# Performance work log

Measured on AMD Instinct MI355X. Metric: run time of the kernel, lower is better.

## Reference

```python
import jax, jax.numpy as jnp
import numpy as np

N_UPDATE = 3

def _lin(key, fan_in, fan_out):
    s = 1.0 / np.sqrt(fan_in)
    k1, k2 = jax.random.split(key)
    W = jax.random.uniform(k1, (fan_in, fan_out), jnp.float32, -s, s)
    b = jax.random.uniform(k2, (fan_out,), jnp.float32, -s, s)
    return W, b

def setup_inputs() -> dict:
    key = jax.random.key(0)
    ks = jax.random.split(key, 12)
    N, E, F_NODE, F_EDGE, H, L, R, T = 50000, 400000, 16, 16, 32, 64, 128, 1
    inp = {}
    inp["x"] = jax.random.normal(ks[0], (N, F_NODE), jnp.float32)
    inp["edge_index"] = jax.random.randint(ks[1], (E, 2), 0, N)  # [E,2] (src,dst)
    inp["edge_attr"] = jax.random.normal(ks[2], (E, F_EDGE), jnp.float32)
    # edge MLP: F_EDGE -> 64 -> 64 -> H*H
    inp["Wm0"], inp["bm0"] = _lin(ks[3], F_EDGE, L)
    inp["Wm1"], inp["bm1"] = _lin(ks[4], L, L)
    inp["Wm2"], inp["bm2"] = _lin(ks[5], L, H * H)
    # NNConv root weight + bias
    inp["root"], inp["bias"] = _lin(ks[6], H, H)
    # readout i-net: 2H -> R -> T ; j-net: H -> R -> T
    inp["Wi0"], inp["bi0"] = _lin(ks[7], 2 * H, R)
    inp["Wi1"], inp["bi1"] = _lin(ks[8], R, T)
    inp["Wj0"], inp["bj0"] = _lin(ks[9], H, R)
    inp["Wj1"], inp["bj1"] = _lin(ks[10], R, T)
    return inp

def reference(x, edge_index, edge_attr, Wm0, bm0, Wm1, bm1, Wm2, bm2,
              root, bias, Wi0, bi0, Wi1, bi1, Wj0, bj0, Wj1, bj1):
    N = x.shape[0]
    H = root.shape[0]
    # h_0 = [x, zeros] padded to hidden_state_size
    h0 = jnp.concatenate([x, jnp.zeros((N, H - x.shape[1]), x.dtype)], axis=1)
    # edge MLP -> per-edge weight matrices (edge_attr constant across updates)
    e = jax.nn.relu(edge_attr @ Wm0 + bm0)
    e = jax.nn.relu(e @ Wm1 + bm1)
    W = (e @ Wm2 + bm2).reshape(-1, H, H)  # [E, H, H]
    src = edge_index[:, 0]
    dst = edge_index[:, 1]
    h = h0
    for _ in range(N_UPDATE):
        msg = jnp.einsum('eh,eho->eo', h[src], W)              # gather + bmm
        agg = jax.ops.segment_sum(msg, dst, num_segments=N)    # scatter-add
        h = h @ root + bias + agg                              # NNConv root/bias
    # mpnn readout: sum_v sigmoid(i([h_T, h_0])) * j(h_T)
    gate = jax.nn.sigmoid(jax.nn.relu(jnp.concatenate([h, h0], 1) @ Wi0 + bi0) @ Wi1 + bi1)
    val = jax.nn.relu(h @ Wj0 + bj0) @ Wj1 + bj1
    return jnp.sum(gate * val, axis=0)  # [target_size]
```

## Files before the change

### kernel.cpp

```cpp
#include <hip/hip_runtime.h>
#include <stdint.h>

#define N_UPDATE 3
#define HD 32
#define FN 16

typedef unsigned short u16;
typedef __bf16 bf16x8 __attribute__((ext_vector_type(8)));
typedef float f32x4 __attribute__((ext_vector_type(4)));

__device__ __forceinline__ float bf2f(u16 u) {
  union { uint32_t i; float f; } v; v.i = ((uint32_t)u) << 16; return v.f;
}
__device__ __forceinline__ u16 f2bf(float f) {
  union { uint32_t i; float f; } v; v.f = f;
  uint32_t x = v.i;
  return (u16)((x + 0x7fffu + ((x >> 16) & 1u)) >> 16);
}

union frag16 { uint4 v; bf16x8 b; u16 s[8]; };

__global__ void k_zero_i(int* __restrict__ p, int n) {
  int i = blockIdx.x * blockDim.x + threadIdx.x;
  if (i < n) p[i] = 0;
}

__global__ void k_hist2(const int* __restrict__ eidx, int* __restrict__ cntS,
                        int* __restrict__ cntD, int E) {
  int e = blockIdx.x * blockDim.x + threadIdx.x;
  if (e >= E) return;
  int2 sd = ((const int2*)eidx)[e];
  atomicAdd(&cntS[sd.x], 1);
  atomicAdd(&cntD[sd.y], 1);
}

__global__ __launch_bounds__(1024) void k_scan(const int* __restrict__ cnt,
                                               int* __restrict__ out1,
                                               int* __restrict__ out2, int N) {
  __shared__ int sums[1024];
  int chunk = (N + 1023) / 1024;
  int beg = threadIdx.x * chunk;
  int end = beg + chunk; if (end > N) end = N;
  if (beg > N) beg = N;
  int s = 0;
  for (int i = beg; i < end; i++) s += cnt[i];
  sums[threadIdx.x] = s;
  __syncthreads();
  for (int off = 1; off < 1024; off <<= 1) {
    int v = (threadIdx.x >= off) ? sums[threadIdx.x - off] : 0;
    __syncthreads();
    sums[threadIdx.x] += v;
    __syncthreads();
  }
  int run = (threadIdx.x == 0) ? 0 : sums[threadIdx.x - 1];
  for (int i = beg; i < end; i++) {
    out1[i] = run;
    if (out2) out2[i] = run;
    run += cnt[i];
  }
  if (end == N) {
    out1[N] = run;
    if (out2) out2[N] = run;
  }
}

__global__ void k_scatter_src(const int* __restrict__ eidx, int* __restrict__ ptrS,
                              int* __restrict__ se_src, int* __restrict__ se_dst,
                              int* __restrict__ invp, int E) {
  int e = blockIdx.x * blockDim.x + threadIdx.x;
  if (e >= E) return;
  int2 sd = ((const int2*)eidx)[e];
  int pos = atomicAdd(&ptrS[sd.x], 1);
  se_src[pos] = sd.x;
  se_dst[pos] = sd.y;
  invp[e] = pos;
}

__global__ void k_dstpos(const int* __restrict__ se_dst, int* __restrict__ ptrD,
                         int* __restrict__ dstpos, int E) {
  int q = blockIdx.x * blockDim.x + threadIdx.x;
  if (q >= E) return;
  dstpos[q] = atomicAdd(&ptrD[se_dst[q]], 1);
}

__global__ void k_prep_bf(const float* __restrict__ Wm2, uint4* __restrict__ Bf) {
  int t = blockIdx.x;
  int lane = threadIdx.x;
  int col = lane & 15;
  int hg = lane >> 4;
  int p = t >> 6;
  int t2 = t & 63;
  int j2 = t2 * 16 + col;
  int o = p * 16 + (j2 >> 6);
  int k = j2 & 63;
  frag16 f;
#pragma unroll
  for (int jj = 0; jj < 8; jj++) {
    int h = hg * 8 + jj;
    f.s[jj] = f2bf(Wm2[k * 1024 + h * 32 + o]);
  }
  Bf[t * 64 + lane] = f.v;
}

__global__ void k_init_h(const float* __restrict__ x, const float* __restrict__ bm2,
                         float* __restrict__ h, float* __restrict__ hbbuf, int N) {
  int idx = blockIdx.x * blockDim.x + threadIdx.x;
  if (idx >= N * HD) return;
  int n = idx >> 5, o = idx & 31;
  float v = (o < FN) ? x[n * FN + o] : 0.f;
  h[idx] = v;
  float hb = 0.f;
#pragma unroll
  for (int k = 0; k < 32; k++)
    hb = fmaf(__shfl(v, k, 32), bm2[k * 32 + o], hb);
  hbbuf[idx] = hb;
}

__global__ __launch_bounds__(256) void k_edge_mlp(
    const float* __restrict__ ea,
    const float* __restrict__ Wm0, const float* __restrict__ bm0,
    const float* __restrict__ Wm1, const float* __restrict__ bm1,
    const int* __restrict__ invp, u16* __restrict__ ee, int E) {
  int e = blockIdx.x * blockDim.x + threadIdx.x;
  if (e >= E) return;
  float a[16];
  {
    const float4* p = (const float4*)(ea + (size_t)e * 16);
    float4 v0 = p[0], v1 = p[1], v2 = p[2], v3 = p[3];
    a[0]=v0.x; a[1]=v0.y; a[2]=v0.z; a[3]=v0.w;
    a[4]=v1.x; a[5]=v1.y; a[6]=v1.z; a[7]=v1.w;
    a[8]=v2.x; a[9]=v2.y; a[10]=v2.z; a[11]=v2.w;
    a[12]=v3.x; a[13]=v3.y; a[14]=v3.z; a[15]=v3.w;
  }
  float t0[64];
#pragma unroll
  for (int j = 0; j < 64; j++) t0[j] = bm0[j];
#pragma unroll
  for (int k = 0; k < 16; k++) {
    float av = a[k];
#pragma unroll
    for (int j = 0; j < 64; j++) t0[j] = fmaf(av, Wm0[k * 64 + j], t0[j]);
  }
#pragma unroll
  for (int j = 0; j < 64; j++) t0[j] = fmaxf(t0[j], 0.f);

  u16* dst = ee + (size_t)invp[e] * 64;
#pragma unroll
  for (int half = 0; half < 2; half++) {
    float t1[32];
#pragma unroll
    for (int j = 0; j < 32; j++) t1[j] = bm1[half * 32 + j];
#pragma unroll
    for (int k = 0; k < 64; k++) {
      float tv = t0[k];
#pragma unroll
      for (int j = 0; j < 32; j++) t1[j] = fmaf(tv, Wm1[k * 64 + half * 32 + j], t1[j]);
    }
    unsigned int out[16];
#pragma unroll
    for (int j = 0; j < 16; j++) {
      u16 lo = f2bf(fmaxf(t1[2 * j], 0.f));
      u16 hi = f2bf(fmaxf(t1[2 * j + 1], 0.f));
      out[j] = (unsigned int)lo | ((unsigned int)hi << 16);
    }
    uint4* op = (uint4*)(dst + half * 32);
#pragma unroll
    for (int q = 0; q < 4; q++) {
      uint4 w; w.x = out[q*4+0]; w.y = out[q*4+1]; w.z = out[q*4+2]; w.w = out[q*4+3];
      op[q] = w;
    }
  }
}

__global__ __launch_bounds__(256) void k_gemm_G(
    const float* __restrict__ h, const uint4* __restrict__ Bf,
    u16* __restrict__ Gb, int N, int p) {
  int wave = threadIdx.x >> 6;
  int lane = threadIdx.x & 63;
  int jt = blockIdx.y * 4 + wave;
  int n0 = blockIdx.x * 16;
  int row = lane & 15;
  int kg = lane >> 4;

  int nr = n0 + row; if (nr > N - 1) nr = N - 1;
  const float* hr = h + (size_t)nr * HD + kg * 8;
  float4 f0 = *(const float4*)hr;
  float4 f1 = *(const float4*)(hr + 4);
  frag16 a;
  a.s[0] = f2bf(f0.x); a.s[1] = f2bf(f0.y); a.s[2] = f2bf(f0.z); a.s[3] = f2bf(f0.w);
  a.s[4] = f2bf(f1.x); a.s[5] = f2bf(f1.y); a.s[6] = f2bf(f1.z); a.s[7] = f2bf(f1.w);

  frag16 b; b.v = Bf[(p * 64 + jt) * 64 + lane];

  f32x4 acc = {0.f, 0.f, 0.f, 0.f};
  acc = __builtin_amdgcn_mfma_f32_16x16x32_bf16(a.b, b.b, acc, 0, 0, 0);

  int j2 = jt * 16 + row;
#pragma unroll
  for (int r = 0; r < 4; r++) {
    int n = n0 + kg * 4 + r;
    if (n < N) Gb[(size_t)n * 1024 + j2] = f2bf(acc[r]);
  }
}

__global__ __launch_bounds__(256) void k_msg(
    const u16* __restrict__ Gb, const float* __restrict__ hbbuf,
    const u16* __restrict__ ee, const int* __restrict__ se_src,
    const int* __restrict__ dstpos, float* __restrict__ msgbuf, int E, int p) {
  int t = blockIdx.x * blockDim.x + threadIdx.x;
  int e = t >> 4;
  int o_l = t & 15;
  if (e >= E) return;
  int src = se_src[e];

  float acc = hbbuf[(size_t)src * HD + p * 16 + o_l];

  const uint4* ep = (const uint4*)(ee + (size_t)e * 64);
  const uint4* gp = (const uint4*)(Gb + ((size_t)src * 16 + o_l) * 64);
  frag16 eu[8], gu[8];
#pragma unroll
  for (int q = 0; q < 8; q++) { eu[q].v = ep[q]; gu[q].v = gp[q]; }
#pragma unroll
  for (int k = 0; k < 64; k++) {
    acc = fmaf(bf2f(eu[k >> 3].s[k & 7]), bf2f(gu[k >> 3].s[k & 7]), acc);
  }
  msgbuf[(size_t)dstpos[e] * HD + p * 16 + o_l] = acc;
}

__global__ __launch_bounds__(256) void k_aggupd(
    const float* __restrict__ msgbuf, const int* __restrict__ rowptrD,
    const float* __restrict__ h, const float* __restrict__ root,
    const float* __restrict__ bias, const float* __restrict__ bm2,
    float* __restrict__ hn, float* __restrict__ hbbuf, int N) {
  int t = blockIdx.x * blockDim.x + threadIdx.x;
  int n = t >> 5, o = t & 31;
  if (n >= N) return;
  int jb = rowptrD[n], je = rowptrD[n + 1];
  float s = 0.f;
  for (int j = jb; j < je; j++) s += msgbuf[(size_t)j * HD + o];

  float hv = h[(size_t)n * HD + o];
  float acc = bias[o] + s;
#pragma unroll
  for (int k = 0; k < 32; k++)
    acc = fmaf(__shfl(hv, k, 32), root[k * HD + o], acc);
  hn[(size_t)n * HD + o] = acc;

  float hb = 0.f;
#pragma unroll
  for (int k = 0; k < 32; k++)
    hb = fmaf(__shfl(acc, k, 32), bm2[k * 32 + o], hb);
  hbbuf[(size_t)n * HD + o] = hb;
}

__global__ __launch_bounds__(256) void k_readout(
    const float* __restrict__ h, const float* __restrict__ x,
    const float* __restrict__ Wi0, const float* __restrict__ bi0,
    const float* __restrict__ Wi1, const float* __restrict__ bi1,
    const float* __restrict__ Wj0, const float* __restrict__ bj0,
    const float* __restrict__ Wj1, const float* __restrict__ bj1,
    float* __restrict__ partial, int N) {
  int wid = threadIdx.x >> 6;
  int lane = threadIdx.x & 63;
  int n = blockIdx.x * 4 + wid;
  __shared__ float sred[4];
  float contrib = 0.f;
  if (n < N) {
    float uv;
    if (lane < 32) uv = h[(size_t)n * HD + lane];
    else if (lane < 48) uv = x[(size_t)n * FN + lane - 32];
    else uv = 0.f;

    float g1a = bi0[lane], g1b = bi0[lane + 64];
#pragma unroll
    for (int k = 0; k < 64; k++) {
      float u = __shfl(uv, k, 64);
      g1a = fmaf(u, Wi0[k * 128 + lane], g1a);
      g1b = fmaf(u, Wi0[k * 128 + lane + 64], g1b);
    }
    g1a = fmaxf(g1a, 0.f); g1b = fmaxf(g1b, 0.f);
    float gp = g1a * Wi1[lane] + g1b * Wi1[lane + 64];

    float v1a = bj0[lane], v1b = bj0[lane + 64];
#pragma unroll
    for (int k = 0; k < 32; k++) {
      float hk = __shfl(uv, k, 64);
      v1a = fmaf(hk, Wj0[k * 128 + lane], v1a);
      v1b = fmaf(hk, Wj0[k * 128 + lane + 64], v1b);
    }
    v1a = fmaxf(v1a, 0.f); v1b = fmaxf(v1b, 0.f);
    float vp = v1a * Wj1[lane] + v1b * Wj1[lane + 64];

#pragma unroll
    for (int s = 32; s; s >>= 1) {
      gp += __shfl_xor(gp, s, 64);
      vp += __shfl_xor(vp, s, 64);
    }
    float gate = 1.f / (1.f + __expf(-(gp + bi1[0])));
    float val = vp + bj1[0];
    contrib = gate * val;
  }
  if (lane == 0) sred[wid] = contrib;
  __syncthreads();
  if (threadIdx.x == 0) partial[blockIdx.x] = sred[0] + sred[1] + sred[2] + sred[3];
}

__global__ void k_final(const float* __restrict__ partial, float* __restrict__ out, int P) {
  __shared__ float sm[256];
  float s = 0.f;
  for (int i = threadIdx.x; i < P; i += 256) s += partial[i];
  sm[threadIdx.x] = s;
  __syncthreads();
  for (int st = 128; st; st >>= 1) {
    if ((int)threadIdx.x < st) sm[threadIdx.x] += sm[threadIdx.x + st];
    __syncthreads();
  }
  if (threadIdx.x == 0) out[0] = sm[0];
}

extern "C" void kernel_launch(void* const* d_in, const int* in_sizes, int n_in,
                              void* d_out, int out_size, void* d_ws, size_t ws_size,
                              hipStream_t stream) {
  const float* x    = (const float*)d_in[0];
  const int*   eidx = (const int*)d_in[1];
  const float* ea   = (const float*)d_in[2];
  const float* Wm0  = (const float*)d_in[3];
  const float* bm0  = (const float*)d_in[4];
  const float* Wm1  = (const float*)d_in[5];
  const float* bm1  = (const float*)d_in[6];
  const float* Wm2  = (const float*)d_in[7];
  const float* bm2  = (const float*)d_in[8];
  const float* root = (const float*)d_in[9];
  const float* bias = (const float*)d_in[10];
  const float* Wi0  = (const float*)d_in[11];
  const float* bi0  = (const float*)d_in[12];
  const float* Wi1  = (const float*)d_in[13];
  const float* bi1  = (const float*)d_in[14];
  const float* Wj0  = (const float*)d_in[15];
  const float* bj0  = (const float*)d_in[16];
  const float* Wj1  = (const float*)d_in[17];
  const float* bj1  = (const float*)d_in[18];

  int N = in_sizes[0] / FN;
  int E = in_sizes[1] / 2;
  int nb = (N + 3) / 4;

  auto al = [](size_t b) { return (b + 255) & ~(size_t)255; };
  size_t need = al((size_t)N * 1024 * 2)
              + al((size_t)E * 64 * 2)
              + al((size_t)E * HD * 4)
              + al(128 * 64 * sizeof(uint4))
              + 3 * al((size_t)N * HD * 4)
              + 2 * al((size_t)N * 4)
              + 3 * al(((size_t)N + 1) * 4)
              + 4 * al((size_t)E * 4)
              + al((size_t)nb * 4);
  if (need > ws_size) return;

  char* ws = (char*)d_ws;
  size_t off = 0;
  auto alloc = [&](size_t bytes) { void* p = ws + off; off += al(bytes); return p; };
  u16*   Gb      = (u16*)alloc((size_t)N * 1024 * 2);
  u16*   ee      = (u16*)alloc((size_t)E * 64 * 2);
  float* msgbuf  = (float*)alloc((size_t)E * HD * 4);
  uint4* Bf      = (uint4*)alloc(128 * 64 * sizeof(uint4));
  float* hA      = (float*)alloc((size_t)N * HD * 4);
  float* hB      = (float*)alloc((size_t)N * HD * 4);
  float* hbbuf   = (float*)alloc((size_t)N * HD * 4);
  int*   cntS    = (int*)alloc((size_t)N * 4);
  int*   cntD    = (int*)alloc((size_t)N * 4);
  int*   ptrS    = (int*)alloc(((size_t)N + 1) * 4);
  int*   rowptrD = (int*)alloc(((size_t)N + 1) * 4);
  int*   ptrD    = (int*)alloc(((size_t)N + 1) * 4);
  int*   se_src  = (int*)alloc((size_t)E * 4);
  int*   se_dst  = (int*)alloc((size_t)E * 4);
  int*   invp    = (int*)alloc((size_t)E * 4);
  int*   dstpos  = (int*)alloc((size_t)E * 4);
  float* partial = (float*)alloc((size_t)nb * 4);

  int mt = (N + 15) / 16;
  int ng = (N * HD + 255) / 256;
  int eg = (E + 255) / 256;

  int zn = (int)(((char*)cntD - (char*)cntS) / 4) + N;
  hipLaunchKernelGGL(k_zero_i, dim3((zn + 255) / 256), dim3(256), 0, stream, cntS, zn);
  hipLaunchKernelGGL(k_hist2, dim3(eg), dim3(256), 0, stream, eidx, cntS, cntD, E);
  hipLaunchKernelGGL(k_scan, dim3(1), dim3(1024), 0, stream, cntS, ptrS, (int*)nullptr, N);
  hipLaunchKernelGGL(k_scan, dim3(1), dim3(1024), 0, stream, cntD, rowptrD, ptrD, N);
  hipLaunchKernelGGL(k_scatter_src, dim3(eg), dim3(256), 0, stream,
                     eidx, ptrS, se_src, se_dst, invp, E);
  hipLaunchKernelGGL(k_dstpos, dim3(eg), dim3(256), 0, stream, se_dst, ptrD, dstpos, E);

  hipLaunchKernelGGL(k_prep_bf, dim3(128), dim3(64), 0, stream, Wm2, Bf);
  hipLaunchKernelGGL(k_init_h, dim3(ng), dim3(256), 0, stream, x, bm2, hA, hbbuf, N);
  hipLaunchKernelGGL(k_edge_mlp, dim3(eg), dim3(256), 0, stream,
                     ea, Wm0, bm0, Wm1, bm1, invp, ee, E);

  float* hc = hA; float* hn = hB;
  for (int it = 0; it < N_UPDATE; it++) {
    for (int p = 0; p < 2; p++) {
      hipLaunchKernelGGL(k_gemm_G, dim3(mt, 16), dim3(256), 0, stream, hc, Bf, Gb, N, p);
      hipLaunchKernelGGL(k_msg, dim3(((size_t)E * 16 + 255) / 256), dim3(256), 0, stream,
                         Gb, hbbuf, ee, se_src, dstpos, msgbuf, E, p);
    }
    hipLaunchKernelGGL(k_aggupd, dim3(ng), dim3(256), 0, stream,
                       msgbuf, rowptrD, hc, root, bias, bm2, hn, hbbuf, N);
    float* tmp = hc; hc = hn; hn = tmp;
  }

  hipLaunchKernelGGL(k_readout, dim3(nb), dim3(256), 0, stream,
                     hc, x, Wi0, bi0, Wi1, bi1, Wj0, bj0, Wj1, bj1, partial, N);
  hipLaunchKernelGGL(k_final, dim3(1), dim3(256), 0, stream, partial, (float*)d_out, nb);
}
```

Baseline: 1.686 ms.

## Interleave G layout for coalesced msg loads and merge edge scatter kernels

The G buffer is now stored interleaved, with 8-element chunks of each of the 16 outputs placed side by side. The 16 threads of one edge in k_msg then read adjacent 16-byte chunks instead of 128-byte strided rows, which makes the gather of G coalesced. k_gemm_G now makes each wave loop over 16 column tiles, so the hidden-state fragment is loaded once per block instead of being relaunched over a 16-wide grid dimension. The source and destination scatter kernels are merged into one that writes a packed (src, dstpos) int2, removing a launch and two index arrays at the cost of a second atomic in the same kernel.

Result: faster. 1.455 ms (-13.7%).

```diff
diff --git a/kernel.cpp b/kernel.cpp
--- a/kernel.cpp
+++ b/kernel.cpp
@@ -64,23 +64,16 @@
   }
 }
 
-__global__ void k_scatter_src(const int* __restrict__ eidx, int* __restrict__ ptrS,
-                              int* __restrict__ se_src, int* __restrict__ se_dst,
-                              int* __restrict__ invp, int E) {
+__global__ void k_scatter(const int* __restrict__ eidx, int* __restrict__ ptrS,
+                          int* __restrict__ ptrD, int2* __restrict__ spd,
+                          int* __restrict__ invp, int E) {
   int e = blockIdx.x * blockDim.x + threadIdx.x;
   if (e >= E) return;
   int2 sd = ((const int2*)eidx)[e];
   int pos = atomicAdd(&ptrS[sd.x], 1);
-  se_src[pos] = sd.x;
-  se_dst[pos] = sd.y;
+  int dpos = atomicAdd(&ptrD[sd.y], 1);
+  spd[pos] = make_int2(sd.x, dpos);
   invp[e] = pos;
-}
-
-__global__ void k_dstpos(const int* __restrict__ se_dst, int* __restrict__ ptrD,
-                         int* __restrict__ dstpos, int E) {
-  int q = blockIdx.x * blockDim.x + threadIdx.x;
-  if (q >= E) return;
-  dstpos[q] = atomicAdd(&ptrD[se_dst[q]], 1);
 }
 
 __global__ void k_prep_bf(const float* __restrict__ Wm2, uint4* __restrict__ Bf) {
@@ -177,7 +170,6 @@
     u16* __restrict__ Gb, int N, int p) {
   int wave = threadIdx.x >> 6;
   int lane = threadIdx.x & 63;
-  int jt = blockIdx.y * 4 + wave;
   int n0 = blockIdx.x * 16;
   int row = lane & 15;
   int kg = lane >> 4;
@@ -190,41 +182,49 @@
   a.s[0] = f2bf(f0.x); a.s[1] = f2bf(f0.y); a.s[2] = f2bf(f0.z); a.s[3] = f2bf(f0.w);
   a.s[4] = f2bf(f1.x); a.s[5] = f2bf(f1.y); a.s[6] = f2bf(f1.z); a.s[7] = f2bf(f1.w);
 
-  frag16 b; b.v = Bf[(p * 64 + jt) * 64 + lane];
-
-  f32x4 acc = {0.f, 0.f, 0.f, 0.f};
-  acc = __builtin_amdgcn_mfma_f32_16x16x32_bf16(a.b, b.b, acc, 0, 0, 0);
-
-  int j2 = jt * 16 + row;
-#pragma unroll
-  for (int r = 0; r < 4; r++) {
-    int n = n0 + kg * 4 + r;
-    if (n < N) Gb[(size_t)n * 1024 + j2] = f2bf(acc[r]);
+#pragma unroll
+  for (int i = 0; i < 16; i++) {
+    int jt = wave * 16 + i;
+    frag16 b; b.v = Bf[(p * 64 + jt) * 64 + lane];
+    f32x4 acc = {0.f, 0.f, 0.f, 0.f};
+    acc = __builtin_amdgcn_mfma_f32_16x16x32_bf16(a.b, b.b, acc, 0, 0, 0);
+
+    int o_l = jt >> 2;
+    int k = (jt & 3) * 16 + row;
+    int idx = (k >> 3) * 128 + o_l * 8 + (k & 7);
+#pragma unroll
+    for (int r = 0; r < 4; r++) {
+      int n = n0 + kg * 4 + r;
+      if (n < N) Gb[(size_t)n * 1024 + idx] = f2bf(acc[r]);
+    }
   }
 }
 
 __global__ __launch_bounds__(256) void k_msg(
     const u16* __restrict__ Gb, const float* __restrict__ hbbuf,
-    const u16* __restrict__ ee, const int* __restrict__ se_src,
-    const int* __restrict__ dstpos, float* __restrict__ msgbuf, int E, int p) {
+    const u16* __restrict__ ee, const int2* __restrict__ spd,
+    float* __restrict__ msgbuf, int E, int p) {
   int t = blockIdx.x * blockDim.x + threadIdx.x;
   int e = t >> 4;
   int o_l = t & 15;
   if (e >= E) return;
-  int src = se_src[e];
-
-  float acc = hbbuf[(size_t)src * HD + p * 16 + o_l];
+  int2 sp = spd[e];
+
+  float acc = hbbuf[(size_t)sp.x * HD + p * 16 + o_l];
 
   const uint4* ep = (const uint4*)(ee + (size_t)e * 64);
-  const uint4* gp = (const uint4*)(Gb + ((size_t)src * 16 + o_l) * 64);
+  const uint4* gp = (const uint4*)(Gb + (size_t)sp.x * 1024);
   frag16 eu[8], gu[8];
 #pragma unroll
-  for (int q = 0; q < 8; q++) { eu[q].v = ep[q]; gu[q].v = gp[q]; }
+  for (int q = 0; q < 8; q++) {
+    eu[q].v = ep[q];
+    gu[q].v = gp[q * 16 + o_l];
+  }
 #pragma unroll
   for (int k = 0; k < 64; k++) {
     acc = fmaf(bf2f(eu[k >> 3].s[k & 7]), bf2f(gu[k >> 3].s[k & 7]), acc);
   }
-  msgbuf[(size_t)dstpos[e] * HD + p * 16 + o_l] = acc;
+  msgbuf[(size_t)sp.y * HD + p * 16 + o_l] = acc;
 }
 
 __global__ __launch_bounds__(256) void k_aggupd(
@@ -353,7 +353,8 @@
               + 3 * al((size_t)N * HD * 4)
               + 2 * al((size_t)N * 4)
               + 3 * al(((size_t)N + 1) * 4)
-              + 4 * al((size_t)E * 4)
+              + al((size_t)E * 8)
+              + al((size_t)E * 4)
               + al((size_t)nb * 4);
   if (need > ws_size) return;
 
@@ -372,10 +373,8 @@
   int*   ptrS    = (int*)alloc(((size_t)N + 1) * 4);
   int*   rowptrD = (int*)alloc(((size_t)N + 1) * 4);
   int*   ptrD    = (int*)alloc(((size_t)N + 1) * 4);
-  int*   se_src  = (int*)alloc((size_t)E * 4);
-  int*   se_dst  = (int*)alloc((size_t)E * 4);
+  int2*  spd     = (int2*)alloc((size_t)E * 8);
   int*   invp    = (int*)alloc((size_t)E * 4);
-  int*   dstpos  = (int*)alloc((size_t)E * 4);
   float* partial = (float*)alloc((size_t)nb * 4);
 
   int mt = (N + 15) / 16;
@@ -387,9 +386,8 @@
   hipLaunchKernelGGL(k_hist2, dim3(eg), dim3(256), 0, stream, eidx, cntS, cntD, E);
   hipLaunchKernelGGL(k_scan, dim3(1), dim3(1024), 0, stream, cntS, ptrS, (int*)nullptr, N);
   hipLaunchKernelGGL(k_scan, dim3(1), dim3(1024), 0, stream, cntD, rowptrD, ptrD, N);
-  hipLaunchKernelGGL(k_scatter_src, dim3(eg), dim3(256), 0, stream,
-                     eidx, ptrS, se_src, se_dst, invp, E);
-  hipLaunchKernelGGL(k_dstpos, dim3(eg), dim3(256), 0, stream, se_dst, ptrD, dstpos, E);
+  hipLaunchKernelGGL(k_scatter, dim3(eg), dim3(256), 0, stream,
+                     eidx, ptrS, ptrD, spd, invp, E);
 
   hipLaunchKernelGGL(k_prep_bf, dim3(128), dim3(64), 0, stream, Wm2, Bf);
   hipLaunchKernelGGL(k_init_h, dim3(ng), dim3(256), 0, stream, x, bm2, hA, hbbuf, N);
@@ -399,9 +397,9 @@
   float* hc = hA; float* hn = hB;
   for (int it = 0; it < N_UPDATE; it++) {
     for (int p = 0; p < 2; p++) {
-      hipLaunchKernelGGL(k_gemm_G, dim3(mt, 16), dim3(256), 0, stream, hc, Bf, Gb, N, p);
+      hipLaunchKernelGGL(k_gemm_G, dim3(mt), dim3(256), 0, stream, hc, Bf, Gb, N, p);
       hipLaunchKernelGGL(k_msg, dim3(((size_t)E * 16 + 255) / 256), dim3(256), 0, stream,
-                         Gb, hbbuf, ee, se_src, dstpos, msgbuf, E, p);
+                         Gb, hbbuf, ee, spd, msgbuf, E, p);
     }
     hipLaunchKernelGGL(k_aggupd, dim3(ng), dim3(256), 0, stream,
                        msgbuf, rowptrD, hc, root, bias, bm2, hn, hbbuf, N);
```
